# Optimization experiments

Measured on AMD Instinct MI355X. Metric: run time of the kernel, lower is better.

The kernel has to match this reference:

```python
import jax, jax.numpy as jnp
import numpy as np

BITS = 4
MAXQ = (1 << BITS) - 1          # 15
PACK = 32 // BITS               # 8 values per int32
IN_F = 4096
OUT_F = 11008


def setup_inputs() -> dict:
    key = jax.random.key(0)
    k1, k2, k3, k4, k5 = jax.random.split(key, 5)
    x = jax.random.normal(k1, (8, IN_F), dtype=jnp.float32)
    qweight = jax.random.randint(k2, (IN_F // 32 * BITS, OUT_F), 0, 2147483647, dtype=jnp.int32)
    qzeros = jax.random.randint(k3, (1, OUT_F // 32 * BITS), 0, 2147483647, dtype=jnp.int32)
    scales = jax.random.uniform(k4, (1, OUT_F), dtype=jnp.float32, minval=1e-3, maxval=2e-2)
    bias = jax.random.normal(k5, (OUT_F,), dtype=jnp.float32)
    return {"x": x, "qweight": qweight, "qzeros": qzeros, "scales": scales, "bias": bias}


def reference(x, qweight, qzeros, scales, bias):
    # GPTQ-style unpack: each int32 packs PACK values of BITS bits, LSB first.
    shifts = jnp.arange(0, 32, BITS, dtype=jnp.int32)  # wf
    # unpack weights: (IN_F//PACK, OUT_F) -> (IN_F//PACK, PACK, OUT_F) -> (IN_F, OUT_F)
    w = (qweight[:, None, :] >> shifts[None, :, None]) & MAXQ
    w = w.reshape(IN_F, OUT_F).astype(scales.dtype)
    # unpack zeros: (1, OUT_F//PACK) -> (1, OUT_F//PACK, PACK) -> (1, OUT_F), +1 per GPTQ convention
    z = ((qzeros[:, :, None] >> shifts[None, None, :]) & MAXQ) + 1
    z = z.reshape(1, OUT_F).astype(scales.dtype)
    # single quantization group (group_size == infeatures, g_idx all zeros)
    W = scales * (w - z)                      # (IN_F, OUT_F)
    return x @ W + bias
```

## Files before the change

kernel.cpp:

```cpp
#include <hip/hip_runtime.h>

#define IN_F 4096
#define OUT_F 11008
#define M 8
#define S_SLICES 16
#define KPS (IN_F / S_SLICES)
#define RPSL (KPS / 8)
#define STEPS (KPS / 32)

typedef __bf16 bf16x8 __attribute__((ext_vector_type(8)));
typedef float  f32x4  __attribute__((ext_vector_type(4)));
typedef unsigned short us8 __attribute__((ext_vector_type(8)));

__device__ __forceinline__ float trunc_bf(float v) {
    return __uint_as_float(__float_as_uint(v) & 0xffff0000u);
}

__global__ __launch_bounds__(64) void rowsum_kernel(
    const float* __restrict__ x, float* __restrict__ rs)
{
    const int r = blockIdx.x, t = threadIdx.x;
    const float4* xp = (const float4*)(x + (size_t)r * IN_F);
    float s = 0.0f;
#pragma unroll
    for (int c = 0; c < 16; ++c) {
        float4 v = xp[c * 64 + t];
        s += trunc_bf(v.x) + trunc_bf(v.y) + trunc_bf(v.z) + trunc_bf(v.w);
    }
#pragma unroll
    for (int off = 1; off < 64; off <<= 1) s += __shfl_xor(s, off, 64);
    if (t == 0) rs[r] = s;
}

__global__ __launch_bounds__(256) void convert_x_kernel(
    const float* __restrict__ x, unsigned short* __restrict__ xb)
{
    const int idx = blockIdx.x * 256 + threadIdx.x;
    const int r = idx >> 9;
    const int c = (idx & 511) * 8;
    us8 o;
    if (r < M) {
        const float4 v0 = *(const float4*)(x + (size_t)r * IN_F + c);
        const float4 v1 = *(const float4*)(x + (size_t)r * IN_F + c + 4);
        o[0] = (unsigned short)(__float_as_uint(v0.x) >> 16);
        o[1] = (unsigned short)(__float_as_uint(v0.y) >> 16);
        o[2] = (unsigned short)(__float_as_uint(v0.z) >> 16);
        o[3] = (unsigned short)(__float_as_uint(v0.w) >> 16);
        o[4] = (unsigned short)(__float_as_uint(v1.x) >> 16);
        o[5] = (unsigned short)(__float_as_uint(v1.y) >> 16);
        o[6] = (unsigned short)(__float_as_uint(v1.z) >> 16);
        o[7] = (unsigned short)(__float_as_uint(v1.w) >> 16);
    } else {
        o = (us8)0;
    }
    *(us8*)(xb + (size_t)r * IN_F + c) = o;
}

__global__ __launch_bounds__(256) void gptq_mfma_kernel(
    const int* __restrict__ qw,
    const unsigned short* __restrict__ xb,
    float* __restrict__ P)
{
    const int lane = threadIdx.x & 63;
    const int wv   = threadIdx.x >> 6;
    const int t    = lane & 15;
    const int quad = lane >> 4;
    const int col  = (blockIdx.x * 4 + wv) * 16 + t;
    const int i0   = blockIdx.y * RPSL;
    const int kb   = blockIdx.y * KPS;

    int    qv [STEPS];
    bf16x8 afr[STEPS];
    const int* qcol = qw + (size_t)(i0 + quad) * OUT_F + col;
    const unsigned short* xrow = xb + (size_t)t * IN_F + kb + quad * 8;
#pragma unroll
    for (int s = 0; s < STEPS; ++s) {
        qv[s]  = qcol[(size_t)s * 4 * OUT_F];
        afr[s] = *(const bf16x8*)(xrow + s * 32);
    }

    f32x4 acc = {0.f, 0.f, 0.f, 0.f};
#pragma unroll
    for (int s = 0; s < STEPS; ++s) {
        union { unsigned short u[8]; bf16x8 v; } bf;
#pragma unroll
        for (int j = 0; j < 8; ++j) {
            const float f = (float)((qv[s] >> (4 * j)) & 15);
            bf.u[j] = (unsigned short)(__float_as_uint(f) >> 16);
        }
        acc = __builtin_amdgcn_mfma_f32_16x16x32_bf16(afr[s], bf.v, acc, 0, 0, 0);
    }

    const int r0 = quad * 4;
    if (r0 < M) {
        float* Pp = P + (size_t)blockIdx.y * (M * OUT_F);
#pragma unroll
        for (int r = 0; r < 4; ++r)
            Pp[(size_t)(r0 + r) * OUT_F + col] = acc[r];
    }
}

__global__ __launch_bounds__(256) void reduce_kernel(
    const float* __restrict__ P, const float* __restrict__ rs,
    const int* __restrict__ qz, const float* __restrict__ sc,
    const float* __restrict__ bias, float* __restrict__ out)
{
    const int idx = blockIdx.x * 256 + threadIdx.x;
    const int j = idx % OUT_F;
    const int r = idx / OUT_F;

    float acc = 0.0f;
#pragma unroll
    for (int s = 0; s < S_SLICES; ++s)
        acc += P[(size_t)s * M * OUT_F + (size_t)r * OUT_F + j];

    const int zw = qz[j >> 3];
    const float z = (float)(((zw >> ((j & 7) * 4)) & 15) + 1);
    out[(size_t)r * OUT_F + j] = fmaf(sc[j], acc - z * rs[r], bias[j]);
}

extern "C" void kernel_launch(void* const* d_in, const int* in_sizes, int n_in,
                              void* d_out, int out_size, void* d_ws, size_t ws_size,
                              hipStream_t stream) {
    const float* x    = (const float*)d_in[0];
    const int*   qw   = (const int*)d_in[1];
    const int*   qz   = (const int*)d_in[2];
    const float* sc   = (const float*)d_in[3];
    const float* bias = (const float*)d_in[4];
    float* out = (float*)d_out;

    float*          P  = (float*)d_ws;
    unsigned short* xb = (unsigned short*)((char*)d_ws + (8u << 20));
    float*          rs = (float*)((char*)d_ws + (16u << 20));

    hipLaunchKernelGGL(rowsum_kernel, dim3(M), dim3(64), 0, stream, x, rs);
    hipLaunchKernelGGL(convert_x_kernel, dim3(32), dim3(256), 0, stream, x, xb);
    hipLaunchKernelGGL(gptq_mfma_kernel, dim3(OUT_F / 64, S_SLICES), dim3(256), 0, stream,
                       qw, xb, P);
    hipLaunchKernelGGL(reduce_kernel, dim3((M * OUT_F) / 256), dim3(256), 0, stream,
                       P, rs, qz, sc, bias, out);
}
```

Baseline: 90.47 us.

## Fuse GPTQ dequant GEMV into single kernel with in-block split-K reduction

Replaces the four launches (rowsum, x conversion, sliced MFMA, partial-sum reduce) with one kernel. Each block owns 16 output columns, and its four waves split K and reduce through shared memory. The weight subtracts the zero point before conversion to bf16, and x is converted from fp32 inline, so the rowsum and workspace round trip go away. It also adds an XCD-aware tile swizzle. In exchange, each wave issues a long serial chain of 32 MFMAs, the grid has fewer, larger blocks, and numerics change because (w - z) is rounded to bf16.

New measurement: 95.77 us. 5.9% more time.

```diff
diff --git a/kernel.cpp b/kernel.cpp
--- a/kernel.cpp
+++ b/kernel.cpp
@@ -3,120 +3,86 @@
 #define IN_F 4096
 #define OUT_F 11008
 #define M 8
-#define S_SLICES 16
-#define KPS (IN_F / S_SLICES)
-#define RPSL (KPS / 8)
-#define STEPS (KPS / 32)
+#define NWAVE 4
+#define KPW (IN_F / NWAVE)
+#define STEPS (KPW / 32)
 
 typedef __bf16 bf16x8 __attribute__((ext_vector_type(8)));
 typedef float  f32x4  __attribute__((ext_vector_type(4)));
-typedef unsigned short us8 __attribute__((ext_vector_type(8)));
 
-__device__ __forceinline__ float trunc_bf(float v) {
-    return __uint_as_float(__float_as_uint(v) & 0xffff0000u);
-}
+__global__ __launch_bounds__(256, 4) void gptq_fused_kernel(
+    const int*   __restrict__ qw,
+    const float* __restrict__ x,
+    const int*   __restrict__ qz,
+    const float* __restrict__ sc,
+    const float* __restrict__ bias,
+    float*       __restrict__ out)
+{
+    __shared__ float red[NWAVE][M][16];
 
-__global__ __launch_bounds__(64) void rowsum_kernel(
-    const float* __restrict__ x, float* __restrict__ rs)
-{
-    const int r = blockIdx.x, t = threadIdx.x;
-    const float4* xp = (const float4*)(x + (size_t)r * IN_F);
-    float s = 0.0f;
-#pragma unroll
-    for (int c = 0; c < 16; ++c) {
-        float4 v = xp[c * 64 + t];
-        s += trunc_bf(v.x) + trunc_bf(v.y) + trunc_bf(v.z) + trunc_bf(v.w);
-    }
-#pragma unroll
-    for (int off = 1; off < 64; off <<= 1) s += __shfl_xor(s, off, 64);
-    if (t == 0) rs[r] = s;
-}
+    const int bid  = (int)blockIdx.x;
+    const int cpx  = (int)gridDim.x >> 3;
+    const int tile = (bid & 7) * cpx + (bid >> 3);
 
-__global__ __launch_bounds__(256) void convert_x_kernel(
-    const float* __restrict__ x, unsigned short* __restrict__ xb)
-{
-    const int idx = blockIdx.x * 256 + threadIdx.x;
-    const int r = idx >> 9;
-    const int c = (idx & 511) * 8;
-    us8 o;
-    if (r < M) {
-        const float4 v0 = *(const float4*)(x + (size_t)r * IN_F + c);
-        const float4 v1 = *(const float4*)(x + (size_t)r * IN_F + c + 4);
-        o[0] = (unsigned short)(__float_as_uint(v0.x) >> 16);
-        o[1] = (unsigned short)(__float_as_uint(v0.y) >> 16);
-        o[2] = (unsigned short)(__float_as_uint(v0.z) >> 16);
-        o[3] = (unsigned short)(__float_as_uint(v0.w) >> 16);
-        o[4] = (unsigned short)(__float_as_uint(v1.x) >> 16);
-        o[5] = (unsigned short)(__float_as_uint(v1.y) >> 16);
-        o[6] = (unsigned short)(__float_as_uint(v1.z) >> 16);
-        o[7] = (unsigned short)(__float_as_uint(v1.w) >> 16);
-    } else {
-        o = (us8)0;
-    }
-    *(us8*)(xb + (size_t)r * IN_F + c) = o;
-}
-
-__global__ __launch_bounds__(256) void gptq_mfma_kernel(
-    const int* __restrict__ qw,
-    const unsigned short* __restrict__ xb,
-    float* __restrict__ P)
-{
-    const int lane = threadIdx.x & 63;
-    const int wv   = threadIdx.x >> 6;
+    const int lane = (int)threadIdx.x & 63;
+    const int w    = (int)threadIdx.x >> 6;
     const int t    = lane & 15;
     const int quad = lane >> 4;
-    const int col  = (blockIdx.x * 4 + wv) * 16 + t;
-    const int i0   = blockIdx.y * RPSL;
-    const int kb   = blockIdx.y * KPS;
+    const int col  = tile * 16 + t;
+    const int k0   = w * KPW;
 
-    int    qv [STEPS];
-    bf16x8 afr[STEPS];
-    const int* qcol = qw + (size_t)(i0 + quad) * OUT_F + col;
-    const unsigned short* xrow = xb + (size_t)t * IN_F + kb + quad * 8;
+    const float zf = (float)(((qz[col >> 3] >> ((col & 7) * 4)) & 15) + 1);
+
+    int qv[STEPS];
+    const int* qp = qw + (size_t)(k0 / 8 + quad) * OUT_F + col;
+#pragma unroll
+    for (int s = 0; s < STEPS; ++s)
+        qv[s] = qp[(size_t)s * 4 * OUT_F];
+
+    const float* xp = x + (size_t)(t & 7) * IN_F + k0 + quad * 8;
+
+    f32x4 acc = {0.f, 0.f, 0.f, 0.f};
+
 #pragma unroll
     for (int s = 0; s < STEPS; ++s) {
-        qv[s]  = qcol[(size_t)s * 4 * OUT_F];
-        afr[s] = *(const bf16x8*)(xrow + s * 32);
+        union { unsigned int u[4]; bf16x8 v; } a;
+        const float4 v0 = *(const float4*)(xp + s * 32);
+        const float4 v1 = *(const float4*)(xp + s * 32 + 4);
+        a.u[0] = (__float_as_uint(v0.x) >> 16) | (__float_as_uint(v0.y) & 0xffff0000u);
+        a.u[1] = (__float_as_uint(v0.z) >> 16) | (__float_as_uint(v0.w) & 0xffff0000u);
+        a.u[2] = (__float_as_uint(v1.x) >> 16) | (__float_as_uint(v1.y) & 0xffff0000u);
+        a.u[3] = (__float_as_uint(v1.z) >> 16) | (__float_as_uint(v1.w) & 0xffff0000u);
+
+        const unsigned q  = (unsigned)qv[s];
+        const unsigned lo = q & 0x0f0f0f0fu;
+        const unsigned hi = (q >> 4) & 0x0f0f0f0fu;
+        union { unsigned int u[4]; bf16x8 v; } b;
+#pragma unroll
+        for (int p = 0; p < 4; ++p) {
+            const float f0 = (float)((lo >> (8 * p)) & 0xffu) - zf;
+            const float f1 = (float)((hi >> (8 * p)) & 0xffu) - zf;
+            b.u[p] = (__float_as_uint(f0) >> 16) | (__float_as_uint(f1) & 0xffff0000u);
+        }
+
+        acc = __builtin_amdgcn_mfma_f32_16x16x32_bf16(a.v, b.v, acc, 0, 0, 0);
     }
 
-    f32x4 acc = {0.f, 0.f, 0.f, 0.f};
-#pragma unroll
-    for (int s = 0; s < STEPS; ++s) {
-        union { unsigned short u[8]; bf16x8 v; } bf;
-#pragma unroll
-        for (int j = 0; j < 8; ++j) {
-            const float f = (float)((qv[s] >> (4 * j)) & 15);
-            bf.u[j] = (unsigned short)(__float_as_uint(f) >> 16);
-        }
-        acc = __builtin_amdgcn_mfma_f32_16x16x32_bf16(afr[s], bf.v, acc, 0, 0, 0);
-    }
-
-    const int r0 = quad * 4;
-    if (r0 < M) {
-        float* Pp = P + (size_t)blockIdx.y * (M * OUT_F);
+    if (quad < 2) {
 #pragma unroll
         for (int r = 0; r < 4; ++r)
-            Pp[(size_t)(r0 + r) * OUT_F + col] = acc[r];
+            red[w][quad * 4 + r][t] = acc[r];
     }
-}
+    __syncthreads();
 
-__global__ __launch_bounds__(256) void reduce_kernel(
-    const float* __restrict__ P, const float* __restrict__ rs,
-    const int* __restrict__ qz, const float* __restrict__ sc,
-    const float* __restrict__ bias, float* __restrict__ out)
-{
-    const int idx = blockIdx.x * 256 + threadIdx.x;
-    const int j = idx % OUT_F;
-    const int r = idx / OUT_F;
-
-    float acc = 0.0f;
+    if (threadIdx.x < M * 16) {
+        const int r = (int)threadIdx.x >> 4;
+        const int c = (int)threadIdx.x & 15;
+        float sacc = 0.f;
 #pragma unroll
-    for (int s = 0; s < S_SLICES; ++s)
-        acc += P[(size_t)s * M * OUT_F + (size_t)r * OUT_F + j];
-
-    const int zw = qz[j >> 3];
-    const float z = (float)(((zw >> ((j & 7) * 4)) & 15) + 1);
-    out[(size_t)r * OUT_F + j] = fmaf(sc[j], acc - z * rs[r], bias[j]);
+        for (int i = 0; i < NWAVE; ++i) sacc += red[i][r][c];
+        const int j = tile * 16 + c;
+        out[(size_t)r * OUT_F + j] = fmaf(sc[j], sacc, bias[j]);
+    }
 }
 
 extern "C" void kernel_launch(void* const* d_in, const int* in_sizes, int n_in,
@@ -127,16 +93,7 @@
     const int*   qz   = (const int*)d_in[2];
     const float* sc   = (const float*)d_in[3];
     const float* bias = (const float*)d_in[4];
-    float* out = (float*)d_out;
 
-    float*          P  = (float*)d_ws;
-    unsigned short* xb = (unsigned short*)((char*)d_ws + (8u << 20));
-    float*          rs = (float*)((char*)d_ws + (16u << 20));
-
-    hipLaunchKernelGGL(rowsum_kernel, dim3(M), dim3(64), 0, stream, x, rs);
-    hipLaunchKernelGGL(convert_x_kernel, dim3(32), dim3(256), 0, stream, x, xb);
-    hipLaunchKernelGGL(gptq_mfma_kernel, dim3(OUT_F / 64, S_SLICES), dim3(256), 0, stream,
-                       qw, xb, P);
-    hipLaunchKernelGGL(reduce_kernel, dim3((M * OUT_F) / 256), dim3(256), 0, stream,
-                       P, rs, qz, sc, bias, out);
+    hipLaunchKernelGGL(gptq_fused_kernel, dim3(OUT_F / 16), dim3(256), 0, stream,
+                       qw, x, qz, sc, bias, (float*)d_out);
 }
```
